# Optimization experiments

Hardware: AMD Instinct MI355X
Metric: run time of the kernel (lower is better)

## Reference

```python
import jax, jax.numpy as jnp
import numpy as np

B, L, D, T = 32, 2048, 64, 512          # batch, seq_len, input_dim, pred steps
H, EK = 2, 64                           # num_heads, embed_dim_per_head
E = H * EK                              # embed_dim = 128
P = 2                                   # function 'L' -> 2 coefficients
LAT, HID = 64, 64                       # latent_dim, hidden_dim
DIM = 2 * D                             # value dim after cat(X, M)


def setup_inputs() -> dict:
    key = jax.random.key(0)
    ks = jax.random.split(key, 20)
    s = 0.05
    inp = {
        "timesteps": jnp.sort(jax.random.uniform(ks[0], (B, L)), axis=-1),
        "X": jax.random.normal(ks[1], (B, L, D)),
        "M": jax.random.bernoulli(ks[2], 0.5, (B, L, D)).astype(jnp.float32),
        "y_time_steps": jnp.sort(jax.random.uniform(ks[3], (B, T)), axis=-1),
        # time_embedding: Linear(1, E)
        "te_w": jax.random.normal(ks[4], (1, E)) * s,
        "te_b": jax.random.normal(ks[5], (E,)) * s,
        # learned queries (1, P, E)
        "query": jax.random.normal(ks[6], (1, P, E)),
        # query_map / key_map: Linear(E, E), stored (in, out)
        "qm_w": jax.random.normal(ks[7], (E, E)) * s,
        "qm_b": jax.random.normal(ks[8], (E,)) * s,
        "km_w": jax.random.normal(ks[9], (E, E)) * s,
        "km_b": jax.random.normal(ks[10], (E,)) * s,
        # shared attention output head: Linear(2*D*H, LAT)
        "out_w": jax.random.normal(ks[11], (DIM * H, LAT)) * s,
        "out_b": jax.random.normal(ks[12], (LAT,)) * s,
        # decoder (depth=1): Linear(LAT, HID) -> ReLU -> Linear(HID, D)
        "dec_w1": jax.random.normal(ks[13], (LAT, HID)) * s,
        "dec_b1": jax.random.normal(ks[14], (HID,)) * s,
        "dec_w2": jax.random.normal(ks[15], (HID, D)) * s,
        "dec_b2": jax.random.normal(ks[16], (D,)) * s,
    }
    return inp


def _forward(timesteps, X, M, y_time_steps, te_w, te_b, query,
             qm_w, qm_b, km_w, km_b, out_w, out_b,
             dec_w1, dec_b1, dec_w2, dec_b2):
    # learn_time_embedding: Linear(1,E) then sin() on indices i % H == 0
    te = timesteps[..., None] @ te_w + te_b                 # (B, L, E)
    sin_idx = (jnp.arange(E) % H) == 0
    key_emb = jnp.where(sin_idx, jnp.sin(te), te)           # (B, L, E)

    value = jnp.concatenate([X, M], axis=-1)                # (B, L, 2D)
    mask = jnp.concatenate([M, M], axis=-1)                 # (B, L, 2D)

    q = query @ qm_w + qm_b                                 # (1, P, E)
    k = key_emb @ km_w + km_b                               # (B, L, E)
    qh = q.reshape(1, P, H, EK).transpose(0, 2, 1, 3)       # (1, H, P, EK)
    kh = k.reshape(B, L, H, EK).transpose(0, 2, 1, 3)       # (B, H, L, EK)

    scores = jnp.einsum('xhpe,bhle->bhpl', qh, kh) / jnp.sqrt(jnp.float32(EK))
    # score broadcast over value dim + per-feature mask fill (-1e9 as in torch)
    logits = jnp.where(mask[:, None, None, :, :] == 0, -1e9,
                       scores[..., None])                   # (B, H, P, L, 2D)
    p_attn = jax.nn.softmax(logits, axis=-2)                # softmax over L
    x = jnp.einsum('bhpld,bld->bhpd', p_attn, value)        # (B, H, P, 2D)

    x = x.transpose(0, 2, 1, 3).reshape(B, P, H * DIM)      # (B, P, H*2D)
    coeffs = x @ out_w + out_b                              # (B, P, LAT)

    # function 'L': linear-in-time latent trajectory
    z = coeffs[:, 0, :][:, None, :] + y_time_steps[..., None] * coeffs[:, 1, :][:, None, :]  # (B, T, LAT)
    h1 = jax.nn.relu(z @ dec_w1 + dec_b1)
    out = h1 @ dec_w2 + dec_b2                              # (B, T, D)
    return out, coeffs


def reference(timesteps, X, M, y_time_steps, te_w, te_b, query,
              qm_w, qm_b, km_w, km_b, out_w, out_b,
              dec_w1, dec_b1, dec_w2, dec_b2):
    return _forward(timesteps, X, M, y_time_steps, te_w, te_b, query,
                    qm_w, qm_b, km_w, km_b, out_w, out_b,
                    dec_w1, dec_b1, dec_w2, dec_b2)
```

## Files before the change

### kernel.cpp

```cpp
#include <hip/hip_runtime.h>
#include <hip/hip_bf16.h>

#define BB 32
#define LL 2048
#define DD 64
#define TT 512

#define WS_R    0
#define WS_C    512
#define WS_ACC  576
#define ACC_STRIDE 576
#define WS_A    (576 + 32*576)
#define WS_B    (WS_A + 2048)

__global__ void __launch_bounds__(256) k1_prep(
    const float* __restrict__ query,
    const float* __restrict__ qm_w,
    const float* __restrict__ qm_b,
    const float* __restrict__ km_w,
    const float* __restrict__ km_b,
    float* __restrict__ ws) {
  __shared__ float q_lds[2 * 128];
  const int t = threadIdx.x;

  for (int i = t; i < 32 * ACC_STRIDE; i += 256) ws[WS_ACC + i] = 0.f;

  {
    const int p = t >> 7, e = t & 127;
    float acc = qm_b[e];
    for (int i = 0; i < 128; ++i)
      acc += query[p * 128 + i] * qm_w[i * 128 + e];
    q_lds[p * 128 + e] = acc;
  }
  __syncthreads();

  for (int o = t; o < 512; o += 256) {
    const int hp = o >> 7, i = o & 127;
    const int h = hp >> 1, p = hp & 1;
    float acc = 0.f;
    for (int e = 0; e < 64; ++e)
      acc += q_lds[p * 128 + h * 64 + e] * km_w[i * 128 + h * 64 + e];
    ws[WS_R + o] = acc;
  }
  if (t < 4) {
    const int h = t >> 1, p = t & 1;
    float acc = 0.f;
    for (int e = 0; e < 64; ++e)
      acc += q_lds[p * 128 + h * 64 + e] * km_b[h * 64 + e];
    ws[WS_C + t] = acc;
  }
}

__global__ void __launch_bounds__(256) k2_attn(
    const float* __restrict__ ts,
    const float* __restrict__ X,
    const float* __restrict__ M,
    const float* __restrict__ te_w,
    const float* __restrict__ te_b,
    float* __restrict__ ws) {
  __shared__ float tew[128], teb[128], r_lds[512], c_lds[4];
  __shared__ float w_lds[128 * 4];
  __shared__ float red[256 * 18];
  const int t = threadIdx.x;
  const int b = blockIdx.y;
  const int lc = blockIdx.x * 128;

  if (t < 128) { tew[t] = te_w[t]; teb[t] = te_b[t]; }
  r_lds[t] = ws[WS_R + t];
  r_lds[t + 256] = ws[WS_R + t + 256];
  if (t < 4) c_lds[t] = ws[WS_C + t];
  __syncthreads();

  {
    const int ll = t >> 1, pair = t & 1;
    const float tt = ts[(size_t)b * LL + lc + ll];
    float a0 = 0.f, a1 = 0.f;
    const float* r0 = &r_lds[(pair * 2) * 128];
    const float* r1 = &r_lds[(pair * 2 + 1) * 128];
    for (int i = 0; i < 128; i += 2) {
      const float f0 = __sinf(tt * tew[i] + teb[i]);
      const float f1 = tt * tew[i + 1] + teb[i + 1];
      a0 += f0 * r0[i] + f1 * r0[i + 1];
      a1 += f0 * r1[i] + f1 * r1[i + 1];
    }
    w_lds[ll * 4 + pair * 2]     = __expf((a0 + c_lds[pair * 2]) * 0.125f);
    w_lds[ll * 4 + pair * 2 + 1] = __expf((a1 + c_lds[pair * 2 + 1]) * 0.125f);
  }
  __syncthreads();

  const int dpair = t & 31, lr = t >> 5;
  float n[4][2] = {}, dn[4][2] = {}, sx[2] = {};
  const float2* X2 = (const float2*)X;
  const float2* M2 = (const float2*)M;
  const size_t base = ((size_t)b * LL + lc) * 32;
  for (int ll = lr; ll < 128; ll += 8) {
    const float2 xv = X2[base + (size_t)ll * 32 + dpair];
    const float2 mv = M2[base + (size_t)ll * 32 + dpair];
    const float mx0 = mv.x * xv.x, mx1 = mv.y * xv.y;
    sx[0] += xv.x; sx[1] += xv.y;
#pragma unroll
    for (int hp = 0; hp < 4; ++hp) {
      const float w = w_lds[ll * 4 + hp];
      n[hp][0]  += w * mx0;  n[hp][1]  += w * mx1;
      dn[hp][0] += w * mv.x; dn[hp][1] += w * mv.y;
    }
  }

#pragma unroll
  for (int hp = 0; hp < 4; ++hp) {
    red[t * 18 + hp * 2 + 0] = n[hp][0];
    red[t * 18 + hp * 2 + 1] = n[hp][1];
    red[t * 18 + 8 + hp * 2 + 0] = dn[hp][0];
    red[t * 18 + 8 + hp * 2 + 1] = dn[hp][1];
  }
  red[t * 18 + 16] = sx[0];
  red[t * 18 + 17] = sx[1];
  __syncthreads();

  if (t < 32) {
    float* accb = ws + WS_ACC + b * ACC_STRIDE;
    for (int j = 0; j < 18; ++j) {
      float s = 0.f;
#pragma unroll
      for (int r2 = 0; r2 < 8; ++r2) s += red[(r2 * 32 + t) * 18 + j];
      if (j < 8) {
        const int hp = j >> 1, half = j & 1;
        atomicAdd(&accb[hp * 64 + 2 * t + half], s);
      } else if (j < 16) {
        const int j2 = j - 8, hp = j2 >> 1, half = j2 & 1;
        atomicAdd(&accb[256 + hp * 64 + 2 * t + half], s);
      } else {
        atomicAdd(&accb[512 + 2 * t + (j - 16)], s);
      }
    }
  }
}

__global__ void __launch_bounds__(128) k3_coeffs(
    const float* __restrict__ out_w,
    const float* __restrict__ out_b,
    const float* __restrict__ dec_w1,
    const float* __restrict__ dec_b1,
    float* __restrict__ ws,
    float* __restrict__ out) {
  __shared__ float x_lds[2 * 256];
  __shared__ float c_lds[2 * 64];
  const int t = threadIdx.x;
  const int b = blockIdx.x;
  const float* accb = ws + WS_ACC + b * ACC_STRIDE;

  for (int o = t; o < 256; o += 128) {
    const int hp = o >> 6, d = o & 63;
    const int h = hp >> 1, p = hp & 1;
    const float num = accb[hp * 64 + d];
    const float den = accb[256 + hp * 64 + d];
    const float sxv = accb[512 + d];
    float x1, x2;
    if (den > 0.f) { x1 = num / den; x2 = 1.f; }
    else           { x1 = sxv * (1.f / (float)LL); x2 = 0.f; }
    x_lds[p * 256 + h * 128 + d] = x1;
    x_lds[p * 256 + h * 128 + 64 + d] = x2;
  }
  __syncthreads();

  {
    const int p = t >> 6, j = t & 63;
    float acc = out_b[j];
    for (int k = 0; k < 256; ++k)
      acc += x_lds[p * 256 + k] * out_w[k * 64 + j];
    out[(size_t)BB * TT * DD + b * 128 + p * 64 + j] = acc;
    c_lds[p * 64 + j] = acc;
  }
  __syncthreads();

  if (t < 64) {
    const int k = t;
    float a = dec_b1[k], bb = 0.f;
    for (int j = 0; j < 64; ++j) {
      const float w1 = dec_w1[j * 64 + k];
      a  += c_lds[j] * w1;
      bb += c_lds[64 + j] * w1;
    }
    ws[WS_A + b * 64 + k] = a;
    ws[WS_B + b * 64 + k] = bb;
  }
}

__global__ void __launch_bounds__(256) k4_decode(
    const float* __restrict__ yts,
    const float* __restrict__ dec_w2,
    const float* __restrict__ dec_b2,
    const float* __restrict__ ws,
    float* __restrict__ out) {
  __shared__ __align__(16) float w2l[4096];
  __shared__ float h1l[16 * 64];
  __shared__ float Al[64], Bl[64], b2l[64], yl[64];
  const int t = threadIdx.x;
  const int b = blockIdx.y;
  const int t0 = blockIdx.x * 64;

  for (int i = t; i < 4096; i += 256) w2l[i] = dec_w2[i];
  if (t < 64) {
    Al[t]  = ws[WS_A + b * 64 + t];
    Bl[t]  = ws[WS_B + b * 64 + t];
    b2l[t] = dec_b2[t];
    yl[t]  = yts[(size_t)b * TT + t0 + t];
  }
  __syncthreads();

  const int tl = t >> 4, dg = t & 15;
  for (int it = 0; it < 4; ++it) {
    {
      int idx = t;
#pragma unroll
      for (int rr = 0; rr < 4; ++rr, idx += 256) {
        const int tl2 = idx >> 6, k = idx & 63;
        h1l[idx] = fmaxf(Al[k] + yl[it * 16 + tl2] * Bl[k], 0.f);
      }
    }
    __syncthreads();
    {
      float a0 = b2l[dg * 4], a1 = b2l[dg * 4 + 1],
            a2 = b2l[dg * 4 + 2], a3 = b2l[dg * 4 + 3];
      const float4* w4 = (const float4*)w2l;
      const float* h1p = &h1l[tl * 64];
      for (int k = 0; k < 64; ++k) {
        const float h = h1p[k];
        const float4 w = w4[k * 16 + dg];
        a0 += h * w.x; a1 += h * w.y; a2 += h * w.z; a3 += h * w.w;
      }
      const int tg = t0 + it * 16 + tl;
      const size_t off = ((size_t)b * TT + tg) * 64 + dg * 4;
      float4 o; o.x = a0; o.y = a1; o.z = a2; o.w = a3;
      *(float4*)(out + off) = o;
    }
    __syncthreads();
  }
}

extern "C" void kernel_launch(void* const* d_in, const int* in_sizes, int n_in,
                              void* d_out, int out_size, void* d_ws, size_t ws_size,
                              hipStream_t stream) {
  const float* ts     = (const float*)d_in[0];
  const float* X      = (const float*)d_in[1];
  const float* M      = (const float*)d_in[2];
  const float* yts    = (const float*)d_in[3];
  const float* te_w   = (const float*)d_in[4];
  const float* te_b   = (const float*)d_in[5];
  const float* query  = (const float*)d_in[6];
  const float* qm_w   = (const float*)d_in[7];
  const float* qm_b   = (const float*)d_in[8];
  const float* km_w   = (const float*)d_in[9];
  const float* km_b   = (const float*)d_in[10];
  const float* out_w  = (const float*)d_in[11];
  const float* out_b  = (const float*)d_in[12];
  const float* dec_w1 = (const float*)d_in[13];
  const float* dec_b1 = (const float*)d_in[14];
  const float* dec_w2 = (const float*)d_in[15];
  const float* dec_b2 = (const float*)d_in[16];
  float* ws = (float*)d_ws;
  float* out = (float*)d_out;

  k1_prep<<<1, 256, 0, stream>>>(query, qm_w, qm_b, km_w, km_b, ws);
  k2_attn<<<dim3(LL / 128, BB), 256, 0, stream>>>(ts, X, M, te_w, te_b, ws);
  k3_coeffs<<<BB, 128, 0, stream>>>(out_w, out_b, dec_w1, dec_b1, ws, out);
  k4_decode<<<dim3(TT / 64, BB), 256, 0, stream>>>(yts, dec_w2, dec_b2, ws, out);
}
```

Before: 142.8 us.

## Fuse four kernels into two with redundant prep and deterministic partial sums

```diff
diff --git a/kernel.cpp b/kernel.cpp
--- a/kernel.cpp
+++ b/kernel.cpp
@@ -6,69 +6,62 @@
 #define DD 64
 #define TT 512
 
-#define WS_R    0
-#define WS_C    512
-#define WS_ACC  576
-#define ACC_STRIDE 576
-#define WS_A    (576 + 32*576)
-#define WS_B    (WS_A + 2048)
-
-__global__ void __launch_bounds__(256) k1_prep(
+#define NCHUNK 16
+#define PSTRIDE 576
+
+__global__ void __launch_bounds__(256) k_attn(
+    const float* __restrict__ ts,
+    const float* __restrict__ X,
+    const float* __restrict__ M,
+    const float* __restrict__ te_w,
+    const float* __restrict__ te_b,
     const float* __restrict__ query,
     const float* __restrict__ qm_w,
     const float* __restrict__ qm_b,
     const float* __restrict__ km_w,
     const float* __restrict__ km_b,
     float* __restrict__ ws) {
-  __shared__ float q_lds[2 * 128];
+  __shared__ float q_lds[256];
+  __shared__ float r_lds[512], c_lds[4];
+  __shared__ float tew[128], teb[128];
+  __shared__ float w_lds[128 * 4];
+  __shared__ float red[256 * 18];
   const int t = threadIdx.x;
-
-  for (int i = t; i < 32 * ACC_STRIDE; i += 256) ws[WS_ACC + i] = 0.f;
-
+  const int b = blockIdx.y;
+  const int lc = blockIdx.x * 128;
+
+  if (t < 128) { tew[t] = te_w[t]; teb[t] = te_b[t]; }
   {
     const int p = t >> 7, e = t & 127;
     float acc = qm_b[e];
+#pragma unroll 8
     for (int i = 0; i < 128; ++i)
       acc += query[p * 128 + i] * qm_w[i * 128 + e];
-    q_lds[p * 128 + e] = acc;
+    q_lds[t] = acc;
   }
   __syncthreads();
 
   for (int o = t; o < 512; o += 256) {
     const int hp = o >> 7, i = o & 127;
     const int h = hp >> 1, p = hp & 1;
+    const float4* km4 = (const float4*)(km_w + i * 128 + h * 64);
+    const float* qp = &q_lds[p * 128 + h * 64];
     float acc = 0.f;
-    for (int e = 0; e < 64; ++e)
-      acc += q_lds[p * 128 + h * 64 + e] * km_w[i * 128 + h * 64 + e];
-    ws[WS_R + o] = acc;
+#pragma unroll
+    for (int e4 = 0; e4 < 16; ++e4) {
+      const float4 w = km4[e4];
+      acc += qp[e4 * 4] * w.x + qp[e4 * 4 + 1] * w.y +
+             qp[e4 * 4 + 2] * w.z + qp[e4 * 4 + 3] * w.w;
+    }
+    r_lds[o] = acc;
   }
   if (t < 4) {
     const int h = t >> 1, p = t & 1;
     float acc = 0.f;
     for (int e = 0; e < 64; ++e)
       acc += q_lds[p * 128 + h * 64 + e] * km_b[h * 64 + e];
-    ws[WS_C + t] = acc;
-  }
-}
-
-__global__ void __launch_bounds__(256) k2_attn(
-    const float* __restrict__ ts,
-    const float* __restrict__ X,
-    const float* __restrict__ M,
-    const float* __restrict__ te_w,
-    const float* __restrict__ te_b,
-    float* __restrict__ ws) {
-  __shared__ float tew[128], teb[128], r_lds[512], c_lds[4];
-  __shared__ float w_lds[128 * 4];
-  __shared__ float red[256 * 18];
-  const int t = threadIdx.x;
-  const int b = blockIdx.y;
-  const int lc = blockIdx.x * 128;
-
-  if (t < 128) { tew[t] = te_w[t]; teb[t] = te_b[t]; }
-  r_lds[t] = ws[WS_R + t];
-  r_lds[t + 256] = ws[WS_R + t + 256];
-  if (t < 4) c_lds[t] = ws[WS_C + t];
+    c_lds[t] = acc;
+  }
   __syncthreads();
 
   {
@@ -118,43 +111,64 @@
   __syncthreads();
 
   if (t < 32) {
-    float* accb = ws + WS_ACC + b * ACC_STRIDE;
+    float* slot = ws + ((size_t)b * NCHUNK + blockIdx.x) * PSTRIDE;
     for (int j = 0; j < 18; ++j) {
       float s = 0.f;
 #pragma unroll
       for (int r2 = 0; r2 < 8; ++r2) s += red[(r2 * 32 + t) * 18 + j];
       if (j < 8) {
         const int hp = j >> 1, half = j & 1;
-        atomicAdd(&accb[hp * 64 + 2 * t + half], s);
+        slot[hp * 64 + 2 * t + half] = s;
       } else if (j < 16) {
         const int j2 = j - 8, hp = j2 >> 1, half = j2 & 1;
-        atomicAdd(&accb[256 + hp * 64 + 2 * t + half], s);
+        slot[256 + hp * 64 + 2 * t + half] = s;
       } else {
-        atomicAdd(&accb[512 + 2 * t + (j - 16)], s);
+        slot[512 + 2 * t + (j - 16)] = s;
       }
     }
   }
 }
 
-__global__ void __launch_bounds__(128) k3_coeffs(
+__global__ void __launch_bounds__(256) k_dec(
+    const float* __restrict__ yts,
     const float* __restrict__ out_w,
     const float* __restrict__ out_b,
     const float* __restrict__ dec_w1,
     const float* __restrict__ dec_b1,
-    float* __restrict__ ws,
+    const float* __restrict__ dec_w2,
+    const float* __restrict__ dec_b2,
+    const float* __restrict__ ws,
     float* __restrict__ out) {
-  __shared__ float x_lds[2 * 256];
-  __shared__ float c_lds[2 * 64];
+  __shared__ float acc_l[576];
+  __shared__ float x_lds[512];
+  __shared__ float c_lds[128];
+  __shared__ float ABl[128];
+  __shared__ __align__(16) float w2l[4096];
+  __shared__ float h1l[16 * 64];
+  __shared__ float b2l[64], yl[64];
   const int t = threadIdx.x;
-  const int b = blockIdx.x;
-  const float* accb = ws + WS_ACC + b * ACC_STRIDE;
-
-  for (int o = t; o < 256; o += 128) {
-    const int hp = o >> 6, d = o & 63;
+  const int b = blockIdx.y;
+  const int t0 = blockIdx.x * 64;
+
+  for (int i = t; i < 4096; i += 256) w2l[i] = dec_w2[i];
+  {
+    const float* p = ws + (size_t)b * NCHUNK * PSTRIDE;
+    for (int o = t; o < 576; o += 256) {
+      float s = 0.f;
+#pragma unroll
+      for (int c = 0; c < NCHUNK; ++c) s += p[c * PSTRIDE + o];
+      acc_l[o] = s;
+    }
+  }
+  if (t < 64) { b2l[t] = dec_b2[t]; yl[t] = yts[b * TT + t0 + t]; }
+  __syncthreads();
+
+  {
+    const int hp = t >> 6, d = t & 63;
     const int h = hp >> 1, p = hp & 1;
-    const float num = accb[hp * 64 + d];
-    const float den = accb[256 + hp * 64 + d];
-    const float sxv = accb[512 + d];
+    const float num = acc_l[hp * 64 + d];
+    const float den = acc_l[256 + hp * 64 + d];
+    const float sxv = acc_l[512 + d];
     float x1, x2;
     if (den > 0.f) { x1 = num / den; x2 = 1.f; }
     else           { x1 = sxv * (1.f / (float)LL); x2 = 0.f; }
@@ -163,13 +177,14 @@
   }
   __syncthreads();
 
-  {
+  if (t < 128) {
     const int p = t >> 6, j = t & 63;
     float acc = out_b[j];
     for (int k = 0; k < 256; ++k)
       acc += x_lds[p * 256 + k] * out_w[k * 64 + j];
-    out[(size_t)BB * TT * DD + b * 128 + p * 64 + j] = acc;
-    c_lds[p * 64 + j] = acc;
+    c_lds[t] = acc;
+    if (blockIdx.x == 0)
+      out[(size_t)BB * TT * DD + b * 128 + t] = acc;
   }
   __syncthreads();
 
@@ -181,30 +196,8 @@
       a  += c_lds[j] * w1;
       bb += c_lds[64 + j] * w1;
     }
-    ws[WS_A + b * 64 + k] = a;
-    ws[WS_B + b * 64 + k] = bb;
-  }
-}
-
-__global__ void __launch_bounds__(256) k4_decode(
-    const float* __restrict__ yts,
-    const float* __restrict__ dec_w2,
-    const float* __restrict__ dec_b2,
-    const float* __restrict__ ws,
-    float* __restrict__ out) {
-  __shared__ __align__(16) float w2l[4096];
-  __shared__ float h1l[16 * 64];
-  __shared__ float Al[64], Bl[64], b2l[64], yl[64];
-  const int t = threadIdx.x;
-  const int b = blockIdx.y;
-  const int t0 = blockIdx.x * 64;
-
-  for (int i = t; i < 4096; i += 256) w2l[i] = dec_w2[i];
-  if (t < 64) {
-    Al[t]  = ws[WS_A + b * 64 + t];
-    Bl[t]  = ws[WS_B + b * 64 + t];
-    b2l[t] = dec_b2[t];
-    yl[t]  = yts[(size_t)b * TT + t0 + t];
+    ABl[k] = a;
+    ABl[64 + k] = bb;
   }
   __syncthreads();
 
@@ -215,7 +208,7 @@
 #pragma unroll
       for (int rr = 0; rr < 4; ++rr, idx += 256) {
         const int tl2 = idx >> 6, k = idx & 63;
-        h1l[idx] = fmaxf(Al[k] + yl[it * 16 + tl2] * Bl[k], 0.f);
+        h1l[idx] = fmaxf(ABl[k] + yl[it * 16 + tl2] * ABl[64 + k], 0.f);
       }
     }
     __syncthreads();
@@ -261,8 +254,8 @@
   float* ws = (float*)d_ws;
   float* out = (float*)d_out;
 
-  k1_prep<<<1, 256, 0, stream>>>(query, qm_w, qm_b, km_w, km_b, ws);
-  k2_attn<<<dim3(LL / 128, BB), 256, 0, stream>>>(ts, X, M, te_w, te_b, ws);
-  k3_coeffs<<<BB, 128, 0, stream>>>(out_w, out_b, dec_w1, dec_b1, ws, out);
-  k4_decode<<<dim3(TT / 64, BB), 256, 0, stream>>>(yts, dec_w2, dec_b2, ws, out);
+  k_attn<<<dim3(NCHUNK, BB), 256, 0, stream>>>(
+      ts, X, M, te_w, te_b, query, qm_w, qm_b, km_w, km_b, ws);
+  k_dec<<<dim3(TT / 64, BB), 256, 0, stream>>>(
+      yts, out_w, out_b, dec_w1, dec_b1, dec_w2, dec_b2, ws, out);
 }
```

Result: faster. 139.2 us (-2.6%).
